# Kernel optimization log

Measured on AMD Instinct MI355X. Metric: run time of the kernel, lower is better.

Reference implementation:

```python
import jax, jax.numpy as jnp
import numpy as np

N = 50000
E = 600000
D_IN = 128
HID = 128
OUT = 64


def setup_inputs() -> dict:
    key = jax.random.key(0)
    ks = jax.random.split(key, 12)
    x = jax.random.normal(ks[0], (N, D_IN), dtype=jnp.float32)
    edge_index = jax.random.randint(ks[1], (2, E), 0, N, dtype=jnp.int32)
    def lin(k, fan_in, fan_out):
        lim = 1.0 / np.sqrt(fan_in)
        kw, kb = jax.random.split(k)
        W = jax.random.uniform(kw, (fan_in, fan_out), minval=-lim, maxval=lim, dtype=jnp.float32)
        b = jax.random.uniform(kb, (fan_out,), minval=-lim, maxval=lim, dtype=jnp.float32)
        return W, b
    W1, b1 = lin(ks[2], D_IN, HID)
    W2, b2 = lin(ks[3], HID, HID)
    W3, b3 = lin(ks[4], HID, HID)
    fcW, fcb = lin(ks[5], HID, OUT)
    return {"x": x, "edge_index": edge_index, "W1": W1, "b1": b1,
            "W2": W2, "b2": b2, "W3": W3, "b3": b3, "fcW": fcW, "fcb": fcb}


def _gcn_prep(edge_index):
    # add self loops, compute symmetric normalization deg^-1/2 * deg^-1/2
    loop = jnp.arange(N, dtype=edge_index.dtype)
    src = jnp.concatenate([edge_index[0], loop])
    dst = jnp.concatenate([edge_index[1], loop])
    deg = jax.ops.segment_sum(jnp.ones_like(dst, dtype=jnp.float32), dst, num_segments=N)
    dinv = jnp.where(deg > 0, jax.lax.rsqrt(deg), 0.0)
    norm = dinv[src] * dinv[dst]  # [E+N]
    return src, dst, norm


def _gcn_layer(x, src, dst, norm, W, b):
    h = x @ W                      # [N, F_out]
    msg = h[src] * norm[:, None]   # gather + scale, [E+N, F_out]
    agg = jax.ops.segment_sum(msg, dst, num_segments=N)
    return agg + b


def reference(x, edge_index, W1, b1, W2, b2, W3, b3, fcW, fcb):
    src, dst, norm = _gcn_prep(edge_index)
    x = jax.nn.relu(_gcn_layer(x, src, dst, norm, W1, b1))
    x = jax.nn.relu(_gcn_layer(x, src, dst, norm, W2, b2))
    x = jax.nn.relu(_gcn_layer(x, src, dst, norm, W3, b3))
    virtual_node_embedding = x[-1]  # last node's embedding [HID]
    out = virtual_node_embedding @ fcW + fcb  # [OUT]
    return out
```

## Files before the change

### kernel.cpp

```cpp
#include <hip/hip_runtime.h>

#define NF 128
#define OUTF 64

#define M2 1
#define M1 2
#define M0 4

#define CAP_F2 2048
#define CAP_E3 4096
#define CAP_F1 32768
#define CAP_E2 65536
#define CAP_F0 131072
#define CAP_E1 262144


__global__ void k_seed(int* __restrict__ mark, int* __restrict__ F2,
                       int* __restrict__ cnt, int last) {
    if (threadIdx.x == 0) {
        mark[last] = M2;
        F2[0] = last;
        cnt[0] = 1;
    }
}

__global__ void k_mark(const int* __restrict__ src, const int* __restrict__ dst, int E,
                       int* __restrict__ mark, int checkBit, int setBit, int last,
                       int2* __restrict__ Elist, int Ecap, int* __restrict__ eCnt,
                       int* __restrict__ Flist, int Fcap, int* __restrict__ fCnt,
                       const int* __restrict__ selfList, const int* __restrict__ selfCnt,
                       int selfCap)
{
    int i = blockIdx.x * blockDim.x + threadIdx.x;

    if (selfList) {
        int sc = *selfCnt; if (sc > selfCap) sc = selfCap;
        if (i < sc) {
            int v = selfList[i];
            if (!(atomicOr(&mark[v], setBit) & setBit)) {
                int p = atomicAdd(fCnt, 1);
                if (p < Fcap) Flist[p] = v;
            }
        }
    }
    if (i < E) {
        int d = dst[i];
        bool hit = checkBit ? ((mark[d] & checkBit) != 0) : (d == last);
        if (hit) {
            int s = src[i];
            int p = atomicAdd(eCnt, 1);
            if (p < Ecap) Elist[p] = make_int2(s, d);
            if (!(atomicOr(&mark[s], setBit) & setBit)) {
                int q = atomicAdd(fCnt, 1);
                if (q < Fcap) Flist[q] = s;
            }
        }
    }
}

__global__ void k_degm(const int* __restrict__ dst, const int* __restrict__ mark,
                       int* __restrict__ deg, int E) {
    int i = blockIdx.x * blockDim.x + threadIdx.x;
    if (i < E) {
        int d = dst[i];
        if (mark[d]) atomicAdd(&deg[d], 1);
    }
}

__global__ void k_dinvm(const int* __restrict__ mark, const int* __restrict__ deg,
                        float* __restrict__ dinv, int n) {
    int i = blockIdx.x * blockDim.x + threadIdx.x;
    if (i < n && mark[i]) dinv[i] = rsqrtf(1.0f + (float)deg[i]);
}

__global__ __launch_bounds__(256) void k_gemm_rows(
    const int* __restrict__ list, const int* __restrict__ cntPtr, int cap,
    const float* __restrict__ Xin, const float* __restrict__ bias,
    const float* __restrict__ W, const float* __restrict__ dinv,
    const int* __restrict__ mark, int aggBit, int last,
    float* __restrict__ H, float* __restrict__ AGG)
{
    __shared__ float wsm[128][128];
    const int t = threadIdx.x;

    {
        const float4* W4 = (const float4*)W;
        float4* S4 = (float4*)&wsm[0][0];
        #pragma unroll
        for (int it = 0; it < 16; ++it) S4[it * 256 + t] = W4[it * 256 + t];
    }
    __syncthreads();

    int cnt = *cntPtr; if (cnt > cap) cnt = cap;
    const int wave = t >> 6, lane = t & 63;

    for (int base = blockIdx.x * 4; base < cnt; base += gridDim.x * 4) {
        int r = base + wave;
        if (r >= cnt) continue;
        int v = list[r];
        size_t off = (size_t)v * NF;

        float x0, x1;
        if (bias) {
            x0 = fmaxf(Xin[off + lane]      + bias[lane],      0.f);
            x1 = fmaxf(Xin[off + lane + 64] + bias[lane + 64], 0.f);
        } else {
            x0 = Xin[off + lane];
            x1 = Xin[off + lane + 64];
        }

        float a0 = 0.f, a1 = 0.f;
        #pragma unroll 16
        for (int k = 0; k < 64; ++k) {
            float xk = __shfl(x0, k);
            a0 += xk * wsm[k][lane];
            a1 += xk * wsm[k][lane + 64];
        }
        #pragma unroll 16
        for (int k = 0; k < 64; ++k) {
            float xk = __shfl(x1, k);
            a0 += xk * wsm[k + 64][lane];
            a1 += xk * wsm[k + 64][lane + 64];
        }

        H[off + lane]      = a0;
        H[off + lane + 64] = a1;

        bool doAgg = (mark ? ((mark[v] & aggBit) != 0) : false) || (v == last);
        if (doAgg) {
            float di = dinv[v], s2 = di * di;
            AGG[off + lane]      = a0 * s2;
            AGG[off + lane + 64] = a1 * s2;
        }
    }
}

__global__ void k_scat(const int2* __restrict__ list, const int* __restrict__ cntPtr, int cap,
                       const float* __restrict__ dinv, const float* __restrict__ H,
                       float* __restrict__ AGG)
{
    int cnt = *cntPtr; if (cnt > cap) cnt = cap;
    int t = threadIdx.x;
    for (int i = blockIdx.x; i < cnt; i += gridDim.x) {
        int2 e = list[i];
        float w = dinv[e.x] * dinv[e.y];
        atomicAdd(&AGG[(size_t)e.y * NF + t], H[(size_t)e.x * NF + t] * w);
    }
}

__global__ void k_fc(const float* __restrict__ AGG3, const float* __restrict__ b3,
                     const float* __restrict__ fcW, const float* __restrict__ fcb,
                     float* __restrict__ out, int last)
{
    __shared__ float xrow[NF];
    int j = threadIdx.x;
    size_t off = (size_t)last * NF;
    xrow[j]      = fmaxf(AGG3[off + j]      + b3[j],      0.f);
    xrow[j + 64] = fmaxf(AGG3[off + j + 64] + b3[j + 64], 0.f);
    __syncthreads();
    float acc = fcb[j];
    #pragma unroll 16
    for (int k = 0; k < NF; ++k) acc += xrow[k] * fcW[k * OUTF + j];
    out[j] = acc;
}

extern "C" void kernel_launch(void* const* d_in, const int* in_sizes, int n_in,
                              void* d_out, int out_size, void* d_ws, size_t ws_size,
                              hipStream_t stream)
{
    const float* x    = (const float*)d_in[0];
    const int*   ei   = (const int*)d_in[1];
    const float* W1   = (const float*)d_in[2];
    const float* b1   = (const float*)d_in[3];
    const float* W2   = (const float*)d_in[4];
    const float* b2   = (const float*)d_in[5];
    const float* W3   = (const float*)d_in[6];
    const float* b3   = (const float*)d_in[7];
    const float* fcW  = (const float*)d_in[8];
    const float* fcb  = (const float*)d_in[9];
    float* out = (float*)d_out;

    const int n = in_sizes[0] / NF;
    const int E = in_sizes[1] / 2;
    const int* src = ei;
    const int* dst = ei + E;
    const int last = n - 1;

    char* wp = (char*)d_ws;
    auto alloc = [&](size_t bytes) -> void* {
        void* r = (void*)wp;
        wp += (bytes + 255) & ~(size_t)255;
        return r;
    };
    int*   deg  = (int*)alloc((size_t)n * 4);
    int*   mark = (int*)alloc((size_t)n * 4);
    int*   cnt  = (int*)alloc(64 * 4);
    size_t zbytes = (char*)wp - (char*)deg;

    float* dinv = (float*)alloc((size_t)n * 4);
    int*   F2   = (int*) alloc(CAP_F2 * 4);
    int2*  E3   = (int2*)alloc(CAP_E3 * 8);
    int*   F1   = (int*) alloc(CAP_F1 * 4);
    int2*  E2   = (int2*)alloc(CAP_E2 * 8);
    int*   F0   = (int*) alloc(CAP_F0 * 4);
    int2*  E1   = (int2*)alloc(CAP_E1 * 8);
    float* H    = (float*)alloc((size_t)n * NF * 4);
    float* aggA = (float*)alloc((size_t)n * NF * 4);
    float* aggB = (float*)alloc((size_t)n * NF * 4);

    const int B  = 256;
    const int EB = (E + B - 1) / B;
    const int NB = (n + B - 1) / B;

    hipMemsetAsync(deg, 0, zbytes, stream);
    k_seed<<<1, 64, 0, stream>>>(mark, F2, cnt, last);

    k_mark<<<EB, B, 0, stream>>>(src, dst, E, mark, 0,  M2, last,
                                 E3, CAP_E3, &cnt[1], F2, CAP_F2, &cnt[0],
                                 nullptr, nullptr, 0);
    k_mark<<<EB, B, 0, stream>>>(src, dst, E, mark, M2, M1, last,
                                 E2, CAP_E2, &cnt[3], F1, CAP_F1, &cnt[2],
                                 F2, &cnt[0], CAP_F2);
    k_mark<<<EB, B, 0, stream>>>(src, dst, E, mark, M1, M0, last,
                                 E1, CAP_E1, &cnt[5], F0, CAP_F0, &cnt[4],
                                 F1, &cnt[2], CAP_F1);

    k_degm <<<EB, B, 0, stream>>>(dst, mark, deg, E);
    k_dinvm<<<NB, B, 0, stream>>>(mark, deg, dinv, n);

    k_gemm_rows<<<384, B, 0, stream>>>(F0, &cnt[4], CAP_F0, x, nullptr, W1,
                                       dinv, mark, M1, -1, H, aggA);
    k_scat<<<2048, 128, 0, stream>>>(E1, &cnt[5], CAP_E1, dinv, H, aggA);

    k_gemm_rows<<<384, B, 0, stream>>>(F1, &cnt[2], CAP_F1, aggA, b1, W2,
                                       dinv, mark, M2, -1, H, aggB);
    k_scat<<<2048, 128, 0, stream>>>(E2, &cnt[3], CAP_E2, dinv, H, aggB);

    k_gemm_rows<<<384, B, 0, stream>>>(F2, &cnt[0], CAP_F2, aggB, b2, W3,
                                       dinv, nullptr, 0, last, H, aggA);
    k_scat<<<2048, 128, 0, stream>>>(E3, &cnt[1], CAP_E3, dinv, H, aggA);

    k_fc<<<1, 64, 0, stream>>>(aggA, b3, fcW, fcb, out, last);
}
```

Before: 166.7 us.

## Fuse frontier scans with degree count and compute per-edge GEMV with atomic scatter

Replaces the mark/degm/dinvm/gemm_rows/scatter pipeline with three vectorized edge scans that also count degrees, emit self-loop edges and zero only the needed aggregation rows. Per-layer work becomes a per-edge transform-then-scatter GEMV that recomputes the normalization from degrees. The last layer and the final FC are fused into one single-block tail kernel. This removes the F0 frontier and the H buffer and cuts the launch count. In exchange it recomputes the 128x128 product once per edge instead of once per node, which can add a lot of FLOPs on layer 1.

```diff
diff --git a/kernel.cpp b/kernel.cpp
--- a/kernel.cpp
+++ b/kernel.cpp
@@ -5,84 +5,166 @@
 
 #define M2 1
 #define M1 2
-#define M0 4
 
 #define CAP_F2 2048
 #define CAP_E3 4096
 #define CAP_F1 32768
 #define CAP_E2 65536
-#define CAP_F0 131072
 #define CAP_E1 262144
 
 
-__global__ void k_seed(int* __restrict__ mark, int* __restrict__ F2,
-                       int* __restrict__ cnt, int last) {
-    if (threadIdx.x == 0) {
-        mark[last] = M2;
-        F2[0] = last;
-        cnt[0] = 1;
-    }
-}
-
-__global__ void k_mark(const int* __restrict__ src, const int* __restrict__ dst, int E,
-                       int* __restrict__ mark, int checkBit, int setBit, int last,
-                       int2* __restrict__ Elist, int Ecap, int* __restrict__ eCnt,
-                       int* __restrict__ Flist, int Fcap, int* __restrict__ fCnt,
-                       const int* __restrict__ selfList, const int* __restrict__ selfCnt,
-                       int selfCap)
-{
-    int i = blockIdx.x * blockDim.x + threadIdx.x;
-
-    if (selfList) {
-        int sc = *selfCnt; if (sc > selfCap) sc = selfCap;
-        if (i < sc) {
-            int v = selfList[i];
-            if (!(atomicOr(&mark[v], setBit) & setBit)) {
-                int p = atomicAdd(fCnt, 1);
-                if (p < Fcap) Flist[p] = v;
+__global__ void k_scan1(const int* __restrict__ src, const int* __restrict__ dst,
+                        int E, int last, int* __restrict__ mark, int* __restrict__ deg,
+                        int* __restrict__ cnt, int* __restrict__ F2,
+                        int2* __restrict__ E3l, int2* __restrict__ E2l)
+{
+    const int gtid = blockIdx.x * blockDim.x + threadIdx.x;
+    if (gtid == 0) {
+        atomicOr(&mark[last], M2);
+        int q = atomicAdd(&cnt[0], 1);
+        if (q < CAP_F2) F2[q] = last;
+        int r = atomicAdd(&cnt[3], 1);
+        if (r < CAP_E2) E2l[r] = make_int2(last, last);
+        int e = atomicAdd(&cnt[1], 1);
+        if (e < CAP_E3) E3l[e] = make_int2(last, last);
+    }
+
+    auto hit = [&](int d, int i) {
+        atomicAdd(&deg[d], 1);
+        if (d == last) {
+            int s = src[i];
+            int p = atomicAdd(&cnt[1], 1);
+            if (p < CAP_E3) E3l[p] = make_int2(s, d);
+            if (s != last && !(atomicOr(&mark[s], M2) & M2)) {
+                int q = atomicAdd(&cnt[0], 1);
+                if (q < CAP_F2) F2[q] = s;
+                int r = atomicAdd(&cnt[3], 1);
+                if (r < CAP_E2) E2l[r] = make_int2(s, s);
             }
         }
-    }
-    if (i < E) {
-        int d = dst[i];
-        bool hit = checkBit ? ((mark[d] & checkBit) != 0) : (d == last);
-        if (hit) {
+    };
+
+    const int nq = E >> 2;
+    if ((((uintptr_t)dst) & 15) == 0) {
+        if (gtid < nq) {
+            int4 d4 = ((const int4*)dst)[gtid];
+            int i = gtid << 2;
+            hit(d4.x, i); hit(d4.y, i + 1); hit(d4.z, i + 2); hit(d4.w, i + 3);
+        }
+        if (gtid == 0)
+            for (int i = nq << 2; i < E; ++i) hit(dst[i], i);
+    } else {
+        for (int k = 0; k < 4; ++k) {
+            int i = gtid * 4 + k;
+            if (i < E) hit(dst[i], i);
+        }
+    }
+}
+
+__global__ void k_scan2(const int* __restrict__ src, const int* __restrict__ dst,
+                        int E, int* __restrict__ mark, int* __restrict__ cnt,
+                        const int* __restrict__ F2, int* __restrict__ F1,
+                        int2* __restrict__ E2l, int2* __restrict__ E1l)
+{
+    const int gtid = blockIdx.x * blockDim.x + threadIdx.x;
+
+    {
+        int sc = cnt[0]; if (sc > CAP_F2) sc = CAP_F2;
+        if (gtid < sc) {
+            int v = F2[gtid];
+            if (!(atomicOr(&mark[v], M1) & M1)) {
+                int p = atomicAdd(&cnt[2], 1);
+                if (p < CAP_F1) F1[p] = v;
+                int r = atomicAdd(&cnt[5], 1);
+                if (r < CAP_E1) E1l[r] = make_int2(v, v);
+            }
+        }
+    }
+
+    auto hit = [&](int d, int i) {
+        if (mark[d] & M2) {
             int s = src[i];
-            int p = atomicAdd(eCnt, 1);
-            if (p < Ecap) Elist[p] = make_int2(s, d);
-            if (!(atomicOr(&mark[s], setBit) & setBit)) {
-                int q = atomicAdd(fCnt, 1);
-                if (q < Fcap) Flist[q] = s;
+            int p = atomicAdd(&cnt[3], 1);
+            if (p < CAP_E2) E2l[p] = make_int2(s, d);
+            if (!(atomicOr(&mark[s], M1) & M1)) {
+                int q = atomicAdd(&cnt[2], 1);
+                if (q < CAP_F1) F1[q] = s;
+                int r = atomicAdd(&cnt[5], 1);
+                if (r < CAP_E1) E1l[r] = make_int2(s, s);
             }
         }
-    }
-}
-
-__global__ void k_degm(const int* __restrict__ dst, const int* __restrict__ mark,
-                       int* __restrict__ deg, int E) {
-    int i = blockIdx.x * blockDim.x + threadIdx.x;
-    if (i < E) {
-        int d = dst[i];
-        if (mark[d]) atomicAdd(&deg[d], 1);
-    }
-}
-
-__global__ void k_dinvm(const int* __restrict__ mark, const int* __restrict__ deg,
-                        float* __restrict__ dinv, int n) {
-    int i = blockIdx.x * blockDim.x + threadIdx.x;
-    if (i < n && mark[i]) dinv[i] = rsqrtf(1.0f + (float)deg[i]);
-}
-
-__global__ __launch_bounds__(256) void k_gemm_rows(
-    const int* __restrict__ list, const int* __restrict__ cntPtr, int cap,
+    };
+
+    const int nq = E >> 2;
+    if ((((uintptr_t)dst) & 15) == 0) {
+        if (gtid < nq) {
+            int4 d4 = ((const int4*)dst)[gtid];
+            int i = gtid << 2;
+            hit(d4.x, i); hit(d4.y, i + 1); hit(d4.z, i + 2); hit(d4.w, i + 3);
+        }
+        if (gtid == 0)
+            for (int i = nq << 2; i < E; ++i) hit(dst[i], i);
+    } else {
+        for (int k = 0; k < 4; ++k) {
+            int i = gtid * 4 + k;
+            if (i < E) hit(dst[i], i);
+        }
+    }
+}
+
+__global__ void k_scan3(const int* __restrict__ src, const int* __restrict__ dst,
+                        int E, const int* __restrict__ mark, int* __restrict__ cnt,
+                        const int* __restrict__ F1, const int* __restrict__ F2,
+                        int2* __restrict__ E1l,
+                        float* __restrict__ AGG1, float* __restrict__ AGG2)
+{
+    const int gtid = blockIdx.x * blockDim.x + threadIdx.x;
+
+    {
+        int f1 = cnt[2]; if (f1 > CAP_F1) f1 = CAP_F1;
+        if (gtid < f1 * NF)
+            AGG1[(size_t)F1[gtid >> 7] * NF + (gtid & 127)] = 0.f;
+        int f2 = cnt[0]; if (f2 > CAP_F2) f2 = CAP_F2;
+        if (gtid < f2 * NF)
+            AGG2[(size_t)F2[gtid >> 7] * NF + (gtid & 127)] = 0.f;
+    }
+
+    auto hit = [&](int d, int i) {
+        if (mark[d] & M1) {
+            int s = src[i];
+            int p = atomicAdd(&cnt[5], 1);
+            if (p < CAP_E1) E1l[p] = make_int2(s, d);
+        }
+    };
+
+    const int nq = E >> 2;
+    if ((((uintptr_t)dst) & 15) == 0) {
+        if (gtid < nq) {
+            int4 d4 = ((const int4*)dst)[gtid];
+            int i = gtid << 2;
+            hit(d4.x, i); hit(d4.y, i + 1); hit(d4.z, i + 2); hit(d4.w, i + 3);
+        }
+        if (gtid == 0)
+            for (int i = nq << 2; i < E; ++i) hit(dst[i], i);
+    } else {
+        for (int k = 0; k < 4; ++k) {
+            int i = gtid * 4 + k;
+            if (i < E) hit(dst[i], i);
+        }
+    }
+}
+
+__global__ __launch_bounds__(256) void k_gemv(
+    const int2* __restrict__ Elist, const int* __restrict__ cntPtr, int cap,
     const float* __restrict__ Xin, const float* __restrict__ bias,
-    const float* __restrict__ W, const float* __restrict__ dinv,
-    const int* __restrict__ mark, int aggBit, int last,
-    float* __restrict__ H, float* __restrict__ AGG)
+    const float* __restrict__ W, const int* __restrict__ deg,
+    float* __restrict__ AGG)
 {
     __shared__ float wsm[128][128];
+    int ecnt = *cntPtr; if (ecnt > cap) ecnt = cap;
+    if ((int)blockIdx.x * 4 >= ecnt) return;
+
     const int t = threadIdx.x;
-
     {
         const float4* W4 = (const float4*)W;
         float4* S4 = (float4*)&wsm[0][0];
@@ -91,24 +173,18 @@
     }
     __syncthreads();
 
-    int cnt = *cntPtr; if (cnt > cap) cnt = cap;
     const int wave = t >> 6, lane = t & 63;
-
-    for (int base = blockIdx.x * 4; base < cnt; base += gridDim.x * 4) {
-        int r = base + wave;
-        if (r >= cnt) continue;
-        int v = list[r];
-        size_t off = (size_t)v * NF;
-
-        float x0, x1;
+    const int wstride = gridDim.x * 4;
+    for (int e = blockIdx.x * 4 + wave; e < ecnt; e += wstride) {
+        int2 ed = Elist[e];
+        float w = rsqrtf(1.f + (float)deg[ed.x]) * rsqrtf(1.f + (float)deg[ed.y]);
+        size_t so = (size_t)ed.x * NF;
+        float x0 = Xin[so + lane];
+        float x1 = Xin[so + lane + 64];
         if (bias) {
-            x0 = fmaxf(Xin[off + lane]      + bias[lane],      0.f);
-            x1 = fmaxf(Xin[off + lane + 64] + bias[lane + 64], 0.f);
-        } else {
-            x0 = Xin[off + lane];
-            x1 = Xin[off + lane + 64];
-        }
-
+            x0 = fmaxf(x0 + bias[lane],      0.f);
+            x1 = fmaxf(x1 + bias[lane + 64], 0.f);
+        }
         float a0 = 0.f, a1 = 0.f;
         #pragma unroll 16
         for (int k = 0; k < 64; ++k) {
@@ -122,47 +198,73 @@
             a0 += xk * wsm[k + 64][lane];
             a1 += xk * wsm[k + 64][lane + 64];
         }
-
-        H[off + lane]      = a0;
-        H[off + lane + 64] = a1;
-
-        bool doAgg = (mark ? ((mark[v] & aggBit) != 0) : false) || (v == last);
-        if (doAgg) {
-            float di = dinv[v], s2 = di * di;
-            AGG[off + lane]      = a0 * s2;
-            AGG[off + lane + 64] = a1 * s2;
-        }
-    }
-}
-
-__global__ void k_scat(const int2* __restrict__ list, const int* __restrict__ cntPtr, int cap,
-                       const float* __restrict__ dinv, const float* __restrict__ H,
-                       float* __restrict__ AGG)
-{
-    int cnt = *cntPtr; if (cnt > cap) cnt = cap;
-    int t = threadIdx.x;
-    for (int i = blockIdx.x; i < cnt; i += gridDim.x) {
-        int2 e = list[i];
-        float w = dinv[e.x] * dinv[e.y];
-        atomicAdd(&AGG[(size_t)e.y * NF + t], H[(size_t)e.x * NF + t] * w);
-    }
-}
-
-__global__ void k_fc(const float* __restrict__ AGG3, const float* __restrict__ b3,
-                     const float* __restrict__ fcW, const float* __restrict__ fcb,
-                     float* __restrict__ out, int last)
-{
-    __shared__ float xrow[NF];
-    int j = threadIdx.x;
-    size_t off = (size_t)last * NF;
-    xrow[j]      = fmaxf(AGG3[off + j]      + b3[j],      0.f);
-    xrow[j + 64] = fmaxf(AGG3[off + j + 64] + b3[j + 64], 0.f);
-    __syncthreads();
-    float acc = fcb[j];
-    #pragma unroll 16
-    for (int k = 0; k < NF; ++k) acc += xrow[k] * fcW[k * OUTF + j];
-    out[j] = acc;
-}
+        size_t off = (size_t)ed.y * NF;
+        atomicAdd(&AGG[off + lane],      w * a0);
+        atomicAdd(&AGG[off + lane + 64], w * a1);
+    }
+}
+
+__global__ __launch_bounds__(256) void k_tail(
+    const int2* __restrict__ E3l, const int* __restrict__ cntPtr, int cap,
+    const float* __restrict__ AGG2, const float* __restrict__ b2,
+    const float* __restrict__ W3, const float* __restrict__ b3,
+    const float* __restrict__ fcW, const float* __restrict__ fcb,
+    const int* __restrict__ deg, int last, float* __restrict__ out)
+{
+    __shared__ float wsm[128][128];
+    const int t = threadIdx.x;
+    {
+        const float4* W4 = (const float4*)W3;
+        float4* S4 = (float4*)&wsm[0][0];
+        #pragma unroll
+        for (int it = 0; it < 16; ++it) S4[it * 256 + t] = W4[it * 256 + t];
+    }
+    __syncthreads();
+
+    const int wave = t >> 6, lane = t & 63;
+    int e3 = *cntPtr; if (e3 > cap) e3 = cap;
+    const float dl = rsqrtf(1.f + (float)deg[last]);
+
+    float acc0 = 0.f, acc1 = 0.f;
+    for (int e = wave; e < e3; e += 4) {
+        int s = E3l[e].x;
+        float w = rsqrtf(1.f + (float)deg[s]) * dl;
+        size_t so = (size_t)s * NF;
+        float x0 = fmaxf(AGG2[so + lane]      + b2[lane],      0.f);
+        float x1 = fmaxf(AGG2[so + lane + 64] + b2[lane + 64], 0.f);
+        float a0 = 0.f, a1 = 0.f;
+        #pragma unroll 16
+        for (int k = 0; k < 64; ++k) {
+            float xk = __shfl(x0, k);
+            a0 += xk * wsm[k][lane];
+            a1 += xk * wsm[k][lane + 64];
+        }
+        #pragma unroll 16
+        for (int k = 0; k < 64; ++k) {
+            float xk = __shfl(x1, k);
+            a0 += xk * wsm[k + 64][lane];
+            a1 += xk * wsm[k + 64][lane + 64];
+        }
+        acc0 += w * a0;
+        acc1 += w * a1;
+    }
+    __syncthreads();
+    wsm[wave][lane]      = acc0;
+    wsm[wave][lane + 64] = acc1;
+    __syncthreads();
+    if (t < NF) {
+        float s4 = wsm[0][t] + wsm[1][t] + wsm[2][t] + wsm[3][t];
+        wsm[8][t] = fmaxf(s4 + b3[t], 0.f);
+    }
+    __syncthreads();
+    if (t < OUTF) {
+        float acc = fcb[t];
+        #pragma unroll 16
+        for (int k = 0; k < NF; ++k) acc += wsm[8][k] * fcW[k * OUTF + t];
+        out[t] = acc;
+    }
+}
+
 
 extern "C" void kernel_launch(void* const* d_in, const int* in_sizes, int n_in,
                               void* d_out, int out_size, void* d_ws, size_t ws_size,
@@ -197,48 +299,26 @@
     int*   cnt  = (int*)alloc(64 * 4);
     size_t zbytes = (char*)wp - (char*)deg;
 
-    float* dinv = (float*)alloc((size_t)n * 4);
     int*   F2   = (int*) alloc(CAP_F2 * 4);
     int2*  E3   = (int2*)alloc(CAP_E3 * 8);
     int*   F1   = (int*) alloc(CAP_F1 * 4);
     int2*  E2   = (int2*)alloc(CAP_E2 * 8);
-    int*   F0   = (int*) alloc(CAP_F0 * 4);
     int2*  E1   = (int2*)alloc(CAP_E1 * 8);
-    float* H    = (float*)alloc((size_t)n * NF * 4);
-    float* aggA = (float*)alloc((size_t)n * NF * 4);
-    float* aggB = (float*)alloc((size_t)n * NF * 4);
-
-    const int B  = 256;
-    const int EB = (E + B - 1) / B;
-    const int NB = (n + B - 1) / B;
+    float* AGG1 = (float*)alloc((size_t)n * NF * 4);
+    float* AGG2 = (float*)alloc((size_t)n * NF * 4);
 
     hipMemsetAsync(deg, 0, zbytes, stream);
-    k_seed<<<1, 64, 0, stream>>>(mark, F2, cnt, last);
-
-    k_mark<<<EB, B, 0, stream>>>(src, dst, E, mark, 0,  M2, last,
-                                 E3, CAP_E3, &cnt[1], F2, CAP_F2, &cnt[0],
-                                 nullptr, nullptr, 0);
-    k_mark<<<EB, B, 0, stream>>>(src, dst, E, mark, M2, M1, last,
-                                 E2, CAP_E2, &cnt[3], F1, CAP_F1, &cnt[2],
-                                 F2, &cnt[0], CAP_F2);
-    k_mark<<<EB, B, 0, stream>>>(src, dst, E, mark, M1, M0, last,
-                                 E1, CAP_E1, &cnt[5], F0, CAP_F0, &cnt[4],
-                                 F1, &cnt[2], CAP_F1);
-
-    k_degm <<<EB, B, 0, stream>>>(dst, mark, deg, E);
-    k_dinvm<<<NB, B, 0, stream>>>(mark, deg, dinv, n);
-
-    k_gemm_rows<<<384, B, 0, stream>>>(F0, &cnt[4], CAP_F0, x, nullptr, W1,
-                                       dinv, mark, M1, -1, H, aggA);
-    k_scat<<<2048, 128, 0, stream>>>(E1, &cnt[5], CAP_E1, dinv, H, aggA);
-
-    k_gemm_rows<<<384, B, 0, stream>>>(F1, &cnt[2], CAP_F1, aggA, b1, W2,
-                                       dinv, mark, M2, -1, H, aggB);
-    k_scat<<<2048, 128, 0, stream>>>(E2, &cnt[3], CAP_E2, dinv, H, aggB);
-
-    k_gemm_rows<<<384, B, 0, stream>>>(F2, &cnt[0], CAP_F2, aggB, b2, W3,
-                                       dinv, nullptr, 0, last, H, aggA);
-    k_scat<<<2048, 128, 0, stream>>>(E3, &cnt[1], CAP_E3, dinv, H, aggA);
-
-    k_fc<<<1, 64, 0, stream>>>(aggA, b3, fcW, fcb, out, last);
-}
+
+    const int B = 256;
+    const int SB = ((E + 3) / 4 + B - 1) / B;
+
+    k_scan1<<<SB, B, 0, stream>>>(src, dst, E, last, mark, deg, cnt, F2, E3, E2);
+    k_scan2<<<SB, B, 0, stream>>>(src, dst, E, mark, cnt, F2, F1, E2, E1);
+    k_scan3<<<SB, B, 0, stream>>>(src, dst, E, mark, cnt, F1, F2, E1, AGG1, AGG2);
+
+    k_gemv<<<256, B, 0, stream>>>(E1, &cnt[5], CAP_E1, x, nullptr, W1, deg, AGG1);
+    k_gemv<<<64,  B, 0, stream>>>(E2, &cnt[3], CAP_E2, AGG1, b1, W2, deg, AGG2);
+
+    k_tail<<<1, B, 0, stream>>>(E3, &cnt[1], CAP_E3, AGG2, b2, W3, b3,
+                                fcW, fcb, deg, last, out);
+}
```

Result: no change. 166.5 us (-0.1%).
